# Performance work log

Hardware: AMD Instinct MI355X
Metric: run time of the kernel (lower is better)

## Reference

```python
import jax, jax.numpy as jnp
import numpy as np

N = 4096
E = 262144
IN_C = 128
OUT_C = 128
EDGE_D = 16


def setup_inputs() -> dict:
    key = jax.random.key(0)
    k = jax.random.split(key, 8)
    x = jax.random.normal(k[0], (N, IN_C), dtype=jnp.float32)
    edge_index = jax.random.randint(k[1], (2, E), 0, N, dtype=jnp.int64)
    edge_attr = jax.random.normal(k[2], (N, N, EDGE_D), dtype=jnp.float32)
    # nn.Linear params: y = x @ W.T + b; store pre-transposed W for x @ W
    s1 = 1.0 / np.sqrt(IN_C + EDGE_D)
    s2 = 1.0 / np.sqrt(OUT_C)
    W1 = jax.random.uniform(k[3], (IN_C + EDGE_D, OUT_C), jnp.float32, -s1, s1)
    b1 = jax.random.uniform(k[4], (OUT_C,), jnp.float32, -s1, s1)
    W2 = jax.random.uniform(k[5], (OUT_C, OUT_C), jnp.float32, -s2, s2)
    b2 = jax.random.uniform(k[6], (OUT_C,), jnp.float32, -s2, s2)
    return {"x": x, "edge_index": edge_index, "edge_attr": edge_attr,
            "W1": W1, "b1": b1, "W2": W2, "b2": b2}


def reference(x, edge_index, edge_attr, W1, b1, W2, b2):
    row, col = edge_index[0], edge_index[1]
    x_row = x[row]                      # [E, IN_C] gather
    e = edge_attr[row, col]             # [E, EDGE_D] gather from dense NxN table
    h = jnp.concatenate([x_row, e], axis=-1)     # [E, IN_C+EDGE_D]
    h = jax.nn.relu(h @ W1 + b1)                  # [E, OUT_C]
    h = jax.nn.relu(h @ W2 + b2)                  # [E, OUT_C]
    # global_add_pool(out, col): scatter-add edges into node buckets by col
    return jax.ops.segment_sum(h, col, num_segments=x.shape[0])  # [N, OUT_C]
```

## Files before the change

### kernel.cpp

```cpp
#include <hip/hip_runtime.h>
#include <hip/hip_bf16.h>

#define NN 4096
#define IC 128
#define OC 128
#define ED 16
#define EPB 64
#define NT 256
#define NSLOT 16
#define NBLK 512
#define NCPY 8

typedef __bf16 bf16x8 __attribute__((ext_vector_type(8)));
typedef float  f32x16 __attribute__((ext_vector_type(16)));

#define BAR() do { asm volatile("s_waitcnt lgkmcnt(0)" ::: "memory"); \
    __builtin_amdgcn_s_barrier(); \
    __builtin_amdgcn_sched_barrier(0); } while (0)

__device__ __forceinline__ unsigned short bf16u(float f) {
    unsigned int u = __float_as_uint(f);
    u = (u + 0x7FFFu + ((u >> 16) & 1u)) >> 16;
    return (unsigned short)u;
}
__device__ __forceinline__ float bf16tof(unsigned short h) {
    return __uint_as_float(((unsigned int)h) << 16);
}
__device__ __forceinline__ int swzk(int row) { return (row ^ (row >> 3)) & 7; }

__global__ __launch_bounds__(128) void k_xw1(
    const float* __restrict__ x, const float* __restrict__ W1,
    const float* __restrict__ b1, const int* __restrict__ eidx,
    float* __restrict__ xw1b, float* __restrict__ out,
    int* __restrict__ hist8, int E)
{
    __shared__ float xs[8][IC];
    const int t = threadIdx.x;
    const int r0 = blockIdx.x * 8;
    #pragma unroll
    for (int r = 0; r < 8; ++r) xs[r][t] = x[(size_t)(r0 + r) * IC + t];

    const float4 z = make_float4(0.f, 0.f, 0.f, 0.f);
    float4* o4 = (float4*)out;
    o4[blockIdx.x * 256 + t]       = z;
    o4[blockIdx.x * 256 + 128 + t] = z;

    {
        const int e0 = blockIdx.x * 512;
        #pragma unroll
        for (int j = 0; j < 4; ++j) {
            const int k = (2 * blockIdx.x + (j >> 1)) & (NCPY - 1);
            atomicAdd(&hist8[k * 4096 + eidx[E + e0 + t + j * 128]], 1);
        }
    }

    __syncthreads();
    float acc[8];
    const float bb = b1[t];
    #pragma unroll
    for (int r = 0; r < 8; ++r) acc[r] = bb;
    #pragma unroll 4
    for (int k = 0; k < IC; ++k) {
        const float w = W1[(size_t)k * OC + t];
        #pragma unroll
        for (int r = 0; r < 8; ++r) acc[r] = fmaf(xs[r][k], w, acc[r]);
    }
    #pragma unroll
    for (int r = 0; r < 8; ++r) xw1b[(size_t)(r0 + r) * OC + t] = acc[r];
}

__global__ __launch_bounds__(256) void k_scanA(
    const int* __restrict__ hist8, int* __restrict__ binloc,
    int* __restrict__ blocksum)
{
    __shared__ int sb[256];
    const int t = threadIdx.x;
    const int bin = blockIdx.x * 256 + t;
    int s = 0;
    #pragma unroll
    for (int k = 0; k < NCPY; ++k) s += hist8[k * 4096 + bin];
    sb[t] = s;
    __syncthreads();
    if (t == 0) {
        int a = 0;
        for (int i = 0; i < 256; ++i) { const int v = sb[i]; sb[i] = a; a += v; }
        blocksum[blockIdx.x] = a;
    }
    __syncthreads();
    binloc[bin] = sb[t];
}

__global__ __launch_bounds__(256) void k_scanB(
    const int* __restrict__ hist8, const int* __restrict__ binloc,
    const int* __restrict__ blocksum, int* __restrict__ cursor8,
    int* __restrict__ colstart, int E)
{
    __shared__ int baseL;
    const int t = threadIdx.x;
    if (t == 0) {
        int a = 0;
        for (int j = 0; j < (int)blockIdx.x; ++j) a += blocksum[j];
        baseL = a;
    }
    __syncthreads();
    const int bin = blockIdx.x * 256 + t;
    int off = baseL + binloc[bin];
    colstart[bin] = off;
    #pragma unroll
    for (int k = 0; k < NCPY; ++k) {
        cursor8[k * 4096 + bin] = off;
        off += hist8[k * 4096 + bin];
    }
    if (bin == 4095) colstart[4096] = E;
}

__global__ void k_scatter(const int* __restrict__ eidx, int* __restrict__ cursor8,
                          int2* __restrict__ csr, int E) {
    const int i = blockIdx.x * blockDim.x + threadIdx.x;
    const int k = blockIdx.x & (NCPY - 1);
    if (i < E) {
        const int row = eidx[i];
        const int col = eidx[E + i];
        const int pos = atomicAdd(&cursor8[k * 4096 + col], 1);
        csr[pos] = make_int2(row, col);
    }
}

__global__ __launch_bounds__(NT, 2) void k_edge12(
    const int2* __restrict__ csr, const float* __restrict__ eattr,
    const float* __restrict__ xw1b, const float* __restrict__ W1,
    const float* __restrict__ W2, const float* __restrict__ b2,
    const int* __restrict__ colstart, float* __restrict__ out, int E)
{
    extern __shared__ char smem[];
    char*   const h1hi = smem;
    char*   const h1lo = smem + 16384;
    float*  const lacc = (float*)(smem + 32768);
    int*    const srowL = (int*)(smem + 40960);
    int*    const scolL = srowL + 256;

    const int t   = threadIdx.x;
    const int l   = t & 63;
    const int wid = t >> 6;
    const int lm  = l & 31;
    const int hi  = l >> 5;
    const int c2  = wid * 32 + lm;

    bf16x8 w2h[8], w2l[8];
    #pragma unroll
    for (int s = 0; s < 8; ++s) {
        union { unsigned short us[8]; bf16x8 v; } Uh, Ul;
        #pragma unroll
        for (int j = 0; j < 8; ++j) {
            const float w = W2[(size_t)(s * 16 + hi * 8 + j) * OC + c2];
            const unsigned short h = bf16u(w);
            Uh.us[j] = h;
            Ul.us[j] = bf16u(w - bf16tof(h));
        }
        w2h[s] = Uh.v; w2l[s] = Ul.v;
    }
    bf16x8 w1h, w1l;
    {
        union { unsigned short us[8]; bf16x8 v; } Uh, Ul;
        #pragma unroll
        for (int j = 0; j < 8; ++j) {
            const float w = W1[(size_t)(IC + hi * 8 + j) * OC + c2];
            const unsigned short h = bf16u(w);
            Uh.us[j] = h;
            Ul.us[j] = bf16u(w - bf16tof(h));
        }
        w1h = Uh.v; w1l = Ul.v;
    }
    const float b2s = b2[c2];

    #pragma unroll
    for (int i = 0; i < NSLOT * OC / NT; ++i) lacc[t + NT * i] = 0.f;

    const int nper = (E / EPB) / NBLK;
    const int ibb  = blockIdx.x * nper;

    if (t < EPB) {
        const int2 r0v = csr[(size_t)ibb * EPB + t];
        srowL[t] = r0v.x; scolL[t] = r0v.y;
        const int ib1 = (nper > 1) ? 1 : 0;
        const int2 r1v = csr[(size_t)(ibb + ib1) * EPB + t];
        srowL[64 + t] = r1v.x; scolL[64 + t] = r1v.y;
    }
    __syncthreads();
    const int colbase0 = scolL[0];

    float4 pe0a, pe0b, pe1a, pe1b;
    {
        const int r0 = srowL[lm], cc0 = scolL[lm];
        const float* p0 = eattr + ((size_t)r0 * NN + cc0) * ED + hi * 8;
        pe0a = ((const float4*)p0)[0]; pe0b = ((const float4*)p0)[1];
        const int r1 = srowL[32 + lm], cc1 = scolL[32 + lm];
        const float* p1 = eattr + ((size_t)r1 * NN + cc1) * ED + hi * 8;
        pe1a = ((const float4*)p1)[0]; pe1b = ((const float4*)p1)[1];
    }
    int2 pidx;
    {
        const int ib2 = (nper > 2) ? 2 : (nper - 1);
        pidx = (t < EPB) ? csr[(size_t)(ibb + ib2) * EPB + t] : make_int2(0, 0);
    }

    for (int ii = 0; ii < nper; ++ii) {
        const int ib4 = ii & 3;

        bf16x8 ah0, al0, ah1, al1;
        {
            const float f0[8] = { pe0a.x, pe0a.y, pe0a.z, pe0a.w,
                                  pe0b.x, pe0b.y, pe0b.z, pe0b.w };
            const float f1[8] = { pe1a.x, pe1a.y, pe1a.z, pe1a.w,
                                  pe1b.x, pe1b.y, pe1b.z, pe1b.w };
            union { unsigned short us[8]; bf16x8 v; } H0, L0, H1, L1;
            #pragma unroll
            for (int j = 0; j < 8; ++j) {
                unsigned short h = bf16u(f0[j]);
                H0.us[j] = h; L0.us[j] = bf16u(f0[j] - bf16tof(h));
                h = bf16u(f1[j]);
                H1.us[j] = h; L1.us[j] = bf16u(f1[j] - bf16tof(h));
            }
            ah0 = H0.v; al0 = L0.v; ah1 = H1.v; al1 = L1.v;
        }
        f32x16 acc0, acc1;
        #pragma unroll
        for (int reg = 0; reg < 16; ++reg) {
            const int r = (reg & 3) + 8 * (reg >> 2) + 4 * hi;
            acc0[reg] = xw1b[(size_t)srowL[ib4 * 64 + r] * OC + c2];
            acc1[reg] = xw1b[(size_t)srowL[ib4 * 64 + 32 + r] * OC + c2];
        }
        acc0 = __builtin_amdgcn_mfma_f32_32x32x16_bf16(ah0, w1h, acc0, 0, 0, 0);
        acc1 = __builtin_amdgcn_mfma_f32_32x32x16_bf16(ah1, w1h, acc1, 0, 0, 0);
        acc0 = __builtin_amdgcn_mfma_f32_32x32x16_bf16(al0, w1h, acc0, 0, 0, 0);
        acc1 = __builtin_amdgcn_mfma_f32_32x32x16_bf16(al1, w1h, acc1, 0, 0, 0);
        acc0 = __builtin_amdgcn_mfma_f32_32x32x16_bf16(ah0, w1l, acc0, 0, 0, 0);
        acc1 = __builtin_amdgcn_mfma_f32_32x32x16_bf16(ah1, w1l, acc1, 0, 0, 0);
        #pragma unroll
        for (int reg = 0; reg < 16; ++reg) {
            const int r = (reg & 3) + 8 * (reg >> 2) + 4 * hi;
            {
                const float f = fmaxf(acc0[reg], 0.f);
                const unsigned short h = bf16u(f);
                const unsigned short lo = bf16u(f - bf16tof(h));
                const int byt = r * 256 + ((c2 * 2) ^ (swzk(r) << 4));
                *(unsigned short*)(h1hi + byt) = h;
                *(unsigned short*)(h1lo + byt) = lo;
            }
            {
                const int r1 = r + 32;
                const float f = fmaxf(acc1[reg], 0.f);
                const unsigned short h = bf16u(f);
                const unsigned short lo = bf16u(f - bf16tof(h));
                const int byt = r1 * 256 + ((c2 * 2) ^ (swzk(r1) << 4));
                *(unsigned short*)(h1hi + byt) = h;
                *(unsigned short*)(h1lo + byt) = lo;
            }
        }
        if (t < EPB) {
            srowL[((ii + 2) & 3) * 64 + t] = pidx.x;
            scolL[((ii + 2) & 3) * 64 + t] = pidx.y;
        }
        {
            const int iin = (ii + 3 < nper) ? (ii + 3) : (nper - 1);
            pidx = (t < EPB) ? csr[(size_t)(ibb + iin) * EPB + t] : make_int2(0, 0);
        }
        {
            const int jb = (ii + 1) & 3;
            const int r0 = srowL[jb * 64 + lm], cc0 = scolL[jb * 64 + lm];
            const float* p0 = eattr + ((size_t)r0 * NN + cc0) * ED + hi * 8;
            pe0a = ((const float4*)p0)[0]; pe0b = ((const float4*)p0)[1];
            const int r1 = srowL[jb * 64 + 32 + lm], cc1 = scolL[jb * 64 + 32 + lm];
            const float* p1 = eattr + ((size_t)r1 * NN + cc1) * ED + hi * 8;
            pe1a = ((const float4*)p1)[0]; pe1b = ((const float4*)p1)[1];
        }
        BAR();

        {
            f32x16 La0 = (f32x16)(0.0f);
            f32x16 La1 = (f32x16)(0.0f);
            const int arow0 = lm;
            const int arow1 = 32 + lm;
            const int ak0 = swzk(arow0) << 4;
            const int ak1 = swzk(arow1) << 4;
            #pragma unroll
            for (int s = 0; s < 8; ++s) {
                const int kb = s * 32 + hi * 16;
                const bf16x8 aH0 = *(const bf16x8*)(h1hi + arow0 * 256 + (kb ^ ak0));
                const bf16x8 aL0 = *(const bf16x8*)(h1lo + arow0 * 256 + (kb ^ ak0));
                const bf16x8 aH1 = *(const bf16x8*)(h1hi + arow1 * 256 + (kb ^ ak1));
                const bf16x8 aL1 = *(const bf16x8*)(h1lo + arow1 * 256 + (kb ^ ak1));
                La0 = __builtin_amdgcn_mfma_f32_32x32x16_bf16(aH0, w2h[s], La0, 0, 0, 0);
                La1 = __builtin_amdgcn_mfma_f32_32x32x16_bf16(aH1, w2h[s], La1, 0, 0, 0);
                La0 = __builtin_amdgcn_mfma_f32_32x32x16_bf16(aL0, w2h[s], La0, 0, 0, 0);
                La1 = __builtin_amdgcn_mfma_f32_32x32x16_bf16(aL1, w2h[s], La1, 0, 0, 0);
                La0 = __builtin_amdgcn_mfma_f32_32x32x16_bf16(aH0, w2l[s], La0, 0, 0, 0);
                La1 = __builtin_amdgcn_mfma_f32_32x32x16_bf16(aH1, w2l[s], La1, 0, 0, 0);
            }

            #pragma unroll
            for (int p = 0; p < 2; ++p) {
                const int mbase = p * 32 + 4 * hi;
                #pragma unroll
                for (int g = 0; g < 4; ++g) {
                    const int eb = mbase + 8 * g;
                    float sv;
                    {
                        const float a0 = (p == 0) ? La0[4 * g] : La1[4 * g];
                        sv = fmaxf(a0 + b2s, 0.f);
                    }
                    int ccur = scolL[ib4 * 64 + eb];
                    #pragma unroll
                    for (int j = 1; j < 4; ++j) {
                        const float aj = (p == 0) ? La0[4 * g + j] : La1[4 * g + j];
                        const float v = fmaxf(aj + b2s, 0.f);
                        const int c = scolL[ib4 * 64 + eb + j];
                        if (c == ccur) {
                            sv += v;
                        } else {
                            const int slot = ccur - colbase0;
                            if (slot < NSLOT) {
                                if (sv != 0.f) atomicAdd(&lacc[slot * OC + c2], sv);
                            } else {
                                if (sv != 0.f) atomicAdd(&out[(size_t)ccur * OC + c2], sv);
                            }
                            ccur = c; sv = v;
                        }
                    }
                    const int slot = ccur - colbase0;
                    if (slot < NSLOT) {
                        if (sv != 0.f) atomicAdd(&lacc[slot * OC + c2], sv);
                    } else {
                        if (sv != 0.f) atomicAdd(&out[(size_t)ccur * OC + c2], sv);
                    }
                }
            }
        }
        BAR();
    }

    const int blk_e0 = ibb * EPB;
    const int blk_e1 = blk_e0 + nper * EPB;
    #pragma unroll 1
    for (int s = 0; s < NSLOT; ++s) {
        const int c = colbase0 + s;
        if (c >= NN) break;
        const int cs = colstart[c];
        const int ce = colstart[c + 1];
        if (ce <= blk_e0 || cs >= blk_e1) continue;
        if (t < OC) {
            const float v = lacc[s * OC + t];
            if (cs >= blk_e0 && ce <= blk_e1) {
                out[(size_t)c * OC + t] = v;
            } else if (v != 0.f) {
                atomicAdd(&out[(size_t)c * OC + t], v);
            }
        }
    }
}

#define LDS_BYTES 43008

extern "C" void kernel_launch(void* const* d_in, const int* in_sizes, int n_in,
                              void* d_out, int out_size, void* d_ws, size_t ws_size,
                              hipStream_t stream) {
    const float* x    = (const float*)d_in[0];
    const int*   eidx = (const int*)d_in[1];
    const float* ea   = (const float*)d_in[2];
    const float* W1   = (const float*)d_in[3];
    const float* b1   = (const float*)d_in[4];
    const float* W2   = (const float*)d_in[5];
    const float* b2   = (const float*)d_in[6];
    float* out = (float*)d_out;

    const int E = in_sizes[1] / 2;

    char* ws = (char*)d_ws;
    float* xw1b     = (float*)ws;
    int*   hist8    = (int*)(ws + 2097152);
    int*   cursor8  = (int*)(ws + 2097152 + 131072);
    int*   colstart = (int*)(ws + 2097152 + 262144);
    int*   binloc   = (int*)(ws + 2097152 + 294912);
    int*   blocksum = (int*)(ws + 2097152 + 311296);
    int2*  csr      = (int2*)(ws + 2097152 + 327680);

    hipMemsetAsync(hist8, 0, 131072, stream);
    k_xw1<<<NN / 8, 128, 0, stream>>>(x, W1, b1, eidx, xw1b, out, hist8, E);
    k_scanA<<<16, 256, 0, stream>>>(hist8, binloc, blocksum);
    k_scanB<<<16, 256, 0, stream>>>(hist8, binloc, blocksum, cursor8, colstart, E);
    k_scatter<<<(E + 255) / 256, 256, 0, stream>>>(eidx, cursor8, csr, E);

    hipFuncSetAttribute(reinterpret_cast<const void*>(k_edge12),
                        hipFuncAttributeMaxDynamicSharedMemorySize, LDS_BYTES);
    k_edge12<<<NBLK, NT, LDS_BYTES, stream>>>(csr, ea, xw1b, W1, W2, b2,
                                              colstart, out, E);
}
```

Before: 132.0 us.

## Fuse histogram, scans and scatter into one kernel with grid barriers

Replaces the memset plus three separate CSR-building launches (scanA, scanB, scatter) with one persistent 1024-block kernel that uses software grid-wide barriers between the phases. The histogram zeroing moves into k_xw1, and the edge indices are loaded once and kept in registers for both the histogram and the scatter. This is meant to cut launch gaps and a memset. In exchange it depends on all 1024 blocks being resident at the same time for the spin barrier to work, and it adds the cost of atomic spinning.

```diff
diff --git a/kernel.cpp b/kernel.cpp
--- a/kernel.cpp
+++ b/kernel.cpp
@@ -10,6 +10,7 @@
 #define NSLOT 16
 #define NBLK 512
 #define NCPY 8
+#define CSRB 1024
 
 typedef __bf16 bf16x8 __attribute__((ext_vector_type(8)));
 typedef float  f32x16 __attribute__((ext_vector_type(16)));
@@ -28,11 +29,34 @@
 }
 __device__ __forceinline__ int swzk(int row) { return (row ^ (row >> 3)) & 7; }
 
+__device__ __forceinline__ void gsync(int* cnt, int* gen, int nb) {
+    __syncthreads();
+    if (threadIdx.x == 0) {
+        __threadfence();
+        const int my = __hip_atomic_load(gen, __ATOMIC_SEQ_CST,
+                                         __HIP_MEMORY_SCOPE_AGENT);
+        const int arrived = __hip_atomic_fetch_add(cnt, 1, __ATOMIC_SEQ_CST,
+                                                   __HIP_MEMORY_SCOPE_AGENT);
+        if (arrived == nb - 1) {
+            __hip_atomic_store(cnt, 0, __ATOMIC_SEQ_CST,
+                               __HIP_MEMORY_SCOPE_AGENT);
+            __hip_atomic_fetch_add(gen, 1, __ATOMIC_SEQ_CST,
+                                   __HIP_MEMORY_SCOPE_AGENT);
+        } else {
+            while (__hip_atomic_load(gen, __ATOMIC_SEQ_CST,
+                                     __HIP_MEMORY_SCOPE_AGENT) == my) {
+                __builtin_amdgcn_s_sleep(8);
+            }
+        }
+        __threadfence();
+    }
+    __syncthreads();
+}
+
 __global__ __launch_bounds__(128) void k_xw1(
     const float* __restrict__ x, const float* __restrict__ W1,
-    const float* __restrict__ b1, const int* __restrict__ eidx,
-    float* __restrict__ xw1b, float* __restrict__ out,
-    int* __restrict__ hist8, int E)
+    const float* __restrict__ b1, float* __restrict__ xw1b,
+    float* __restrict__ out, int* __restrict__ hist8, int* __restrict__ gbar)
 {
     __shared__ float xs[8][IC];
     const int t = threadIdx.x;
@@ -44,15 +68,10 @@
     float4* o4 = (float4*)out;
     o4[blockIdx.x * 256 + t]       = z;
     o4[blockIdx.x * 256 + 128 + t] = z;
-
-    {
-        const int e0 = blockIdx.x * 512;
-        #pragma unroll
-        for (int j = 0; j < 4; ++j) {
-            const int k = (2 * blockIdx.x + (j >> 1)) & (NCPY - 1);
-            atomicAdd(&hist8[k * 4096 + eidx[E + e0 + t + j * 128]], 1);
-        }
-    }
+    if (blockIdx.x < 64)
+        ((int4*)hist8)[blockIdx.x * 128 + t] = make_int4(0, 0, 0, 0);
+    if (blockIdx.x == 64 && t < 2)
+        gbar[t] = 0;
 
     __syncthreads();
     float acc[8];
@@ -69,60 +88,63 @@
     for (int r = 0; r < 8; ++r) xw1b[(size_t)(r0 + r) * OC + t] = acc[r];
 }
 
-__global__ __launch_bounds__(256) void k_scanA(
-    const int* __restrict__ hist8, int* __restrict__ binloc,
-    int* __restrict__ blocksum)
+__global__ __launch_bounds__(256) void k_csr(
+    const int* __restrict__ eidx, int* __restrict__ hist8,
+    int* __restrict__ binloc, int* __restrict__ blocksum,
+    int* __restrict__ cursor8, int* __restrict__ colstart,
+    int2* __restrict__ csr, int* __restrict__ gbar, int E)
 {
     __shared__ int sb[256];
-    const int t = threadIdx.x;
-    const int bin = blockIdx.x * 256 + t;
-    int s = 0;
-    #pragma unroll
-    for (int k = 0; k < NCPY; ++k) s += hist8[k * 4096 + bin];
-    sb[t] = s;
-    __syncthreads();
-    if (t == 0) {
-        int a = 0;
-        for (int i = 0; i < 256; ++i) { const int v = sb[i]; sb[i] = a; a += v; }
-        blocksum[blockIdx.x] = a;
-    }
-    __syncthreads();
-    binloc[bin] = sb[t];
-}
-
-__global__ __launch_bounds__(256) void k_scanB(
-    const int* __restrict__ hist8, const int* __restrict__ binloc,
-    const int* __restrict__ blocksum, int* __restrict__ cursor8,
-    int* __restrict__ colstart, int E)
-{
-    __shared__ int baseL;
-    const int t = threadIdx.x;
-    if (t == 0) {
-        int a = 0;
-        for (int j = 0; j < (int)blockIdx.x; ++j) a += blocksum[j];
-        baseL = a;
-    }
-    __syncthreads();
-    const int bin = blockIdx.x * 256 + t;
-    int off = baseL + binloc[bin];
-    colstart[bin] = off;
-    #pragma unroll
-    for (int k = 0; k < NCPY; ++k) {
-        cursor8[k * 4096 + bin] = off;
-        off += hist8[k * 4096 + bin];
-    }
-    if (bin == 4095) colstart[4096] = E;
-}
-
-__global__ void k_scatter(const int* __restrict__ eidx, int* __restrict__ cursor8,
-                          int2* __restrict__ csr, int E) {
-    const int i = blockIdx.x * blockDim.x + threadIdx.x;
-    const int k = blockIdx.x & (NCPY - 1);
+    const int t   = threadIdx.x;
+    const int bid = blockIdx.x;
+    const int i   = bid * 256 + t;
+    const int k   = bid & (NCPY - 1);
+
+    const int myrow = (i < E) ? eidx[i] : 0;
+    const int mycol = (i < E) ? eidx[E + i] : 0;
+    if (i < E) atomicAdd(&hist8[k * 4096 + mycol], 1);
+    gsync(gbar, gbar + 1, CSRB);
+
+    if (bid < 16) {
+        const int bin = bid * 256 + t;
+        int s = 0;
+        #pragma unroll
+        for (int c = 0; c < NCPY; ++c) s += hist8[c * 4096 + bin];
+        sb[t] = s;
+        __syncthreads();
+        if (t == 0) {
+            int a = 0;
+            for (int j = 0; j < 256; ++j) { const int v = sb[j]; sb[j] = a; a += v; }
+            blocksum[bid] = a;
+        }
+        __syncthreads();
+        binloc[bin] = sb[t];
+    }
+    gsync(gbar, gbar + 1, CSRB);
+
+    if (bid < 16) {
+        __shared__ int baseL;
+        if (t == 0) {
+            int a = 0;
+            for (int j = 0; j < bid; ++j) a += blocksum[j];
+            baseL = a;
+        }
+        __syncthreads();
+        const int bin = bid * 256 + t;
+        int off = baseL + binloc[bin];
+        colstart[bin] = off;
+        #pragma unroll
+        for (int c = 0; c < NCPY; ++c) {
+            cursor8[c * 4096 + bin] = off;
+            off += hist8[c * 4096 + bin];
+        }
+        if (bin == 4095) colstart[4096] = E;
+    }
+    gsync(gbar, gbar + 1, CSRB);
+
     if (i < E) {
-        const int row = eidx[i];
-        const int col = eidx[E + i];
-        const int pos = atomicAdd(&cursor8[k * 4096 + col], 1);
-        csr[pos] = make_int2(row, col);
+        const int pos = atomicAdd(&cursor8[k * 4096 + mycol], 1);
+        csr[pos] = make_int2(myrow, mycol);
     }
 }
 
@@ -382,13 +404,12 @@
     int*   colstart = (int*)(ws + 2097152 + 262144);
     int*   binloc   = (int*)(ws + 2097152 + 294912);
     int*   blocksum = (int*)(ws + 2097152 + 311296);
+    int*   gbar     = (int*)(ws + 2097152 + 315392);
     int2*  csr      = (int2*)(ws + 2097152 + 327680);
 
-    hipMemsetAsync(hist8, 0, 131072, stream);
-    k_xw1<<<NN / 8, 128, 0, stream>>>(x, W1, b1, eidx, xw1b, out, hist8, E);
-    k_scanA<<<16, 256, 0, stream>>>(hist8, binloc, blocksum);
-    k_scanB<<<16, 256, 0, stream>>>(hist8, binloc, blocksum, cursor8, colstart, E);
-    k_scatter<<<(E + 255) / 256, 256, 0, stream>>>(eidx, cursor8, csr, E);
+    k_xw1<<<NN / 8, 128, 0, stream>>>(x, W1, b1, xw1b, out, hist8, gbar);
+    k_csr<<<CSRB, 256, 0, stream>>>(eidx, hist8, binloc, blocksum,
+                                    cursor8, colstart, csr, gbar, E);
 
     hipFuncSetAttribute(reinterpret_cast<const void*>(k_edge12),
                         hipFuncAttributeMaxDynamicSharedMemorySize, LDS_BYTES);
```

After: 454.0 us. 3.44x slower.
